# Kernel tuning notes

Hardware: AMD Instinct MI355X
Metric: run time of the kernel (lower is better)

The kernel has to match this reference:

```python
import jax, jax.numpy as jnp
import numpy as np

N_HEAD = 12

def setup_inputs() -> dict:
    key = jax.random.key(0)
    k1, k2, k3, k4, k5 = jax.random.split(key, 5)
    B, T, C = 2, 2048, 768
    x = jax.random.normal(k1, (B, T, C), dtype=jnp.float32)
    W_attn = jax.random.normal(k2, (C, 3 * C), dtype=jnp.float32) * 0.02
    b_attn = jax.random.normal(k3, (3 * C,), dtype=jnp.float32) * 0.02
    W_proj = jax.random.normal(k4, (C, C), dtype=jnp.float32) * 0.02
    b_proj = jax.random.normal(k5, (C,), dtype=jnp.float32) * 0.02
    return {"x": x, "W_attn": W_attn, "b_attn": b_attn, "W_proj": W_proj, "b_proj": b_proj}

def reference(x, W_attn, b_attn, W_proj, b_proj):
    B, T, C = x.shape
    H = N_HEAD
    hd = C // H
    qkv = x @ W_attn + b_attn  # [B,T,3C]
    q, k, v = jnp.split(qkv, 3, axis=2)
    # [B,H,T,hd]
    q = q.reshape(B, T, H, hd).transpose(0, 2, 1, 3)
    k = k.reshape(B, T, H, hd).transpose(0, 2, 1, 3)
    v = v.reshape(B, T, H, hd).transpose(0, 2, 1, 3)
    att = jnp.einsum('bhqd,bhkd->bhqk', q, k) / jnp.sqrt(jnp.float32(hd))
    causal = jnp.tril(jnp.ones((T, T), dtype=bool))
    att = jnp.where(causal[None, None], att, -jnp.inf)
    att = jax.nn.softmax(att, axis=-1)
    y = jnp.einsum('bhqk,bhkd->bhqd', att, v)  # [B,H,T,hd]
    y = y.transpose(0, 2, 1, 3).reshape(B, T, C)
    return y @ W_proj + b_proj
```

## Files before the change

kernel.cpp:

```cpp
#include <hip/hip_runtime.h>
#include <stdint.h>

typedef unsigned short u16;
typedef __attribute__((ext_vector_type(8))) short bf16x8;
typedef __attribute__((ext_vector_type(4))) float f32x4;

__device__ __forceinline__ u16 f2bf(float f){
  union { float f; uint32_t u; } v; v.f = f;
  uint32_t u = v.u;
  u += 0x7FFFu + ((u >> 16) & 1u);
  return (u16)(u >> 16);
}

__device__ __forceinline__ float fexp2(float x){
#if __has_builtin(__builtin_amdgcn_exp2f)
  return __builtin_amdgcn_exp2f(x);
#else
  return exp2f(x);
#endif
}

__device__ __forceinline__ uint32_t cvtpk_bf16(float lo, float hi){
  uint32_t d;
  asm("v_cvt_pk_bf16_f32 %0, %1, %2" : "=v"(d) : "v"(lo), "v"(hi));
  return d;
}

__device__ __forceinline__ f32x4 mfma_bf16(bf16x8 a, bf16x8 b, f32x4 c){
  return __builtin_amdgcn_mfma_f32_16x16x32_bf16(a, b, c, 0, 0, 0);
}

#define QSCALE 0.1803368801111244f

__global__ __launch_bounds__(256) void cast_x_k(const float* __restrict__ x,
                                                u16* __restrict__ xb, int n4){
  int i = blockIdx.x*256 + threadIdx.x;
  if (i >= n4) return;
  float4 v = reinterpret_cast<const float4*>(x)[i];
  uint2 o;
  o.x = (uint32_t)f2bf(v.x) | ((uint32_t)f2bf(v.y) << 16);
  o.y = (uint32_t)f2bf(v.z) | ((uint32_t)f2bf(v.w) << 16);
  reinterpret_cast<uint2*>(xb)[i] = o;
}

__global__ __launch_bounds__(256) void transpose_cast_k(const float* __restrict__ in,
                                                        u16* __restrict__ out,
                                                        int R, int C){
  __shared__ u16 tile[64][66];
  int c0 = blockIdx.x*64, r0 = blockIdx.y*64;
  int tc = threadIdx.x & 63, t4 = threadIdx.x >> 6;
  #pragma unroll
  for (int i=0;i<16;i++){ int r = t4 + i*4; tile[r][tc] = f2bf(in[(size_t)(r0+r)*C + c0 + tc]); }
  __syncthreads();
  #pragma unroll
  for (int i=0;i<16;i++){ int cc = t4 + i*4; out[(size_t)(c0+cc)*R + r0 + tc] = tile[tc][cc]; }
}

#define LDP 40

template<int MFRAG>
__global__ __launch_bounds__(256) void gemm_bf16_k(
    const u16* __restrict__ A, const u16* __restrict__ Bt,
    int M, int N, int K, const float* __restrict__ bias, int mode,
    u16* __restrict__ qo, u16* __restrict__ ko, u16* __restrict__ vo,
    float* __restrict__ fo)
{
  constexpr int BM = MFRAG*32;
  __shared__ u16 As[BM*LDP];
  __shared__ u16 Bs[128*LDP];
  const int m0 = blockIdx.y*BM, n0 = blockIdx.x*128;
  const int tid = threadIdx.x, lane = tid & 63, wid = tid >> 6;
  const int lr = lane & 15, lg = lane >> 4;
  const int wr = wid >> 1, wc = wid & 1;
  f32x4 acc[MFRAG][4] = {};
  const int nk = K >> 5;
  for (int kk = 0; kk < nk; ++kk){
    #pragma unroll
    for (int s = 0; s < MFRAG/2; ++s){
      int ci = tid + 256*s;
      int row = ci >> 2, ch = ci & 3;
      *(uint4*)&As[row*LDP + ch*8] = *(const uint4*)&A[(size_t)(m0+row)*K + kk*32 + ch*8];
    }
    #pragma unroll
    for (int s = 0; s < 2; ++s){
      int ci = tid + 256*s;
      int row = ci >> 2, ch = ci & 3;
      *(uint4*)&Bs[row*LDP + ch*8] = *(const uint4*)&Bt[(size_t)(n0+row)*K + kk*32 + ch*8];
    }
    __syncthreads();
    bf16x8 af[MFRAG], bfr[4];
    #pragma unroll
    for (int m=0;m<MFRAG;m++) af[m] = *(const bf16x8*)&As[(wr*(MFRAG*16) + m*16 + lr)*LDP + lg*8];
    #pragma unroll
    for (int n=0;n<4;n++) bfr[n] = *(const bf16x8*)&Bs[(wc*64 + n*16 + lr)*LDP + lg*8];
    #pragma unroll
    for (int m=0;m<MFRAG;m++)
      #pragma unroll
      for (int n=0;n<4;n++)
        acc[m][n] = mfma_bf16(af[m], bfr[n], acc[m][n]);
    __syncthreads();
  }
  if (mode == 0){
    #pragma unroll
    for (int m=0;m<MFRAG;m++)
      #pragma unroll
      for (int n=0;n<4;n++){
        int gn = n0 + wc*64 + n*16 + lr;
        float bv = bias[gn];
        #pragma unroll
        for (int r=0;r<4;r++){
          int gm = m0 + wr*(MFRAG*16) + m*16 + lg*4 + r;
          fo[(size_t)gm*N + gn] = acc[m][n][r] + bv;
        }
      }
  } else {
    int which = n0 / 768;
    u16* dst = (which==0) ? qo : ko;
    float sc = (which==0) ? QSCALE : 1.0f;
    #pragma unroll
    for (int m=0;m<MFRAG;m++)
      #pragma unroll
      for (int n=0;n<4;n++){
        int gn = n0 + wc*64 + n*16 + lr;
        float bv = bias[gn];
        int cn = gn - which*768;
        int h = cn >> 6, d = cn & 63;
        int gm0 = m0 + wr*(MFRAG*16) + m*16 + lg*4;
        int b = gm0 >> 11, t0 = gm0 & 2047;
        if (which < 2){
          #pragma unroll
          for (int r=0;r<4;r++)
            dst[(size_t)((b*12 + h)*2048 + t0 + r)*64 + d] = f2bf((acc[m][n][r] + bv)*sc);
        } else {
          uint2 o;
          o.x = cvtpk_bf16(acc[m][n][0]+bv, acc[m][n][1]+bv);
          o.y = cvtpk_bf16(acc[m][n][2]+bv, acc[m][n][3]+bv);
          *(uint2*)&vo[((size_t)((b*12 + h)*64 + d))*2048 + t0] = o;
        }
      }
  }
}

__global__ __launch_bounds__(256) void attn_k(
    const u16* __restrict__ qp, const u16* __restrict__ kp,
    const u16* __restrict__ vtp, u16* __restrict__ yp)
{
  __shared__ f32x4 ylh[16][64];
  __shared__ float llh[4][16];
  const int i = blockIdx.x;
  const int bh = i % 24;
  const int qsb = 31 - (i / 24);
  const int q0 = qsb * 64;
  const int b = bh / 12, h = bh - b*12;
  const size_t base = (size_t)bh * 131072;
  const int tid = threadIdx.x, lane = tid & 63, wid = tid >> 6;
  const int lr = lane & 15, lg = lane >> 4;
  const u16* kbase = kp + base;
  const u16* vbase = vtp + base;

  bf16x8 qf0[2], qf1[2], qf2[2], qf3[2];
  #pragma unroll
  for (int kb=0;kb<2;kb++){
    qf0[kb] = *(const bf16x8*)&qp[base + (size_t)(q0      + lr)*64 + kb*32 + lg*8];
    qf1[kb] = *(const bf16x8*)&qp[base + (size_t)(q0 + 16 + lr)*64 + kb*32 + lg*8];
    qf2[kb] = *(const bf16x8*)&qp[base + (size_t)(q0 + 32 + lr)*64 + kb*32 + lg*8];
    qf3[kb] = *(const bf16x8*)&qp[base + (size_t)(q0 + 48 + lr)*64 + kb*32 + lg*8];
  }

  f32x4 y0[4] = {}, y1[4] = {}, y2[4] = {}, y3[4] = {};
  float l0 = 0.f, l1 = 0.f, l2 = 0.f, l3 = 0.f;
  const float m2 = 8.f;
  const int nt = qsb + 1;

  uint32_t ko[8], vo[8];
  #pragma unroll
  for (int nb=0;nb<4;nb++){
    int ke = ((nb&1)*32 + (lr>>2)*8 + (nb>>1)*4 + (lr&3))*64 + lg*8;
    ko[nb*2+0] = (uint32_t)(wid*4096 + ke) * 2u;
    ko[nb*2+1] = (uint32_t)(wid*4096 + ke + 32) * 2u;
  }
  #pragma unroll
  for (int n=0;n<4;n++){
    int ve = (n*16+lr)*2048 + lg*8 + wid*64;
    vo[n*2+0] = (uint32_t)ve * 2u;
    vo[n*2+1] = (uint32_t)(ve + 32) * 2u;
  }

  for (int t = wid; t < nt; t += 4){
    bf16x8 kf[8], vf[8];
    #pragma unroll
    for (int j=0;j<8;j++) kf[j] = *(const bf16x8*)((const char*)kbase + ko[j]);
    #pragma unroll
    for (int j=0;j<8;j++) vf[j] = *(const bf16x8*)((const char*)vbase + vo[j]);
    #pragma unroll
    for (int j=0;j<8;j++){ ko[j] += 32768u; vo[j] += 512u; }

    const int k0 = t*64;
    const int nbmin[4] = {0, 32, 4, 36};

    auto do_half = [&](int q0H, const bf16x8 (&qfH)[2], f32x4 (&yH)[4], float &lH){
      const int qgH = q0H + lr;
      f32x4 s[4] = {};
      __builtin_amdgcn_s_setprio(1);
      if (k0      <= q0H + 15){ s[0]=mfma_bf16(kf[0],qfH[0],s[0]); s[0]=mfma_bf16(kf[1],qfH[1],s[0]); }
      if (k0 + 32 <= q0H + 15){ s[1]=mfma_bf16(kf[2],qfH[0],s[1]); s[1]=mfma_bf16(kf[3],qfH[1],s[1]); }
      if (k0 +  4 <= q0H + 15){ s[2]=mfma_bf16(kf[4],qfH[0],s[2]); s[2]=mfma_bf16(kf[5],qfH[1],s[2]); }
      if (k0 + 36 <= q0H + 15){ s[3]=mfma_bf16(kf[6],qfH[0],s[3]); s[3]=mfma_bf16(kf[7],qfH[1],s[3]); }
      __builtin_amdgcn_s_setprio(0);
      if (k0 + 63 > q0H){
        #pragma unroll
        for (int nb=0;nb<4;nb++){
          int kb0 = k0 + (nb&1)*32 + ((nb>>1)&1)*4 + lg*8;
          #pragma unroll
          for (int r=0;r<4;r++)
            if (kb0 + r > qgH) s[nb][r] = -1e30f;
        }
      }
      float lsum = 0.f;
      #pragma unroll
      for (int nb=0;nb<4;nb++){
        if (k0 + nbmin[nb] <= q0H + 15){
          #pragma unroll
          for (int r=0;r<4;r++){
            float p = fexp2(s[nb][r] - m2);
            s[nb][r] = p;
            lsum += p;
          }
        } else {
          #pragma unroll
          for (int r=0;r<4;r++) s[nb][r] = 0.f;
        }
      }
      lH += lsum;
      uint32_t pk[8];
      #pragma unroll
      for (int nb=0;nb<4;nb++){
        pk[nb*2]   = cvtpk_bf16(s[nb][0], s[nb][1]);
        pk[nb*2+1] = cvtpk_bf16(s[nb][2], s[nb][3]);
      }
      __builtin_amdgcn_s_setprio(1);
      union { uint32_t u[4]; bf16x8 v; } pb;
      pb.u[0]=pk[0]; pb.u[1]=pk[1]; pb.u[2]=pk[4]; pb.u[3]=pk[5];
      yH[0]=mfma_bf16(vf[0],pb.v,yH[0]); yH[1]=mfma_bf16(vf[2],pb.v,yH[1]);
      yH[2]=mfma_bf16(vf[4],pb.v,yH[2]); yH[3]=mfma_bf16(vf[6],pb.v,yH[3]);
      pb.u[0]=pk[2]; pb.u[1]=pk[3]; pb.u[2]=pk[6]; pb.u[3]=pk[7];
      yH[0]=mfma_bf16(vf[1],pb.v,yH[0]); yH[1]=mfma_bf16(vf[3],pb.v,yH[1]);
      yH[2]=mfma_bf16(vf[5],pb.v,yH[2]); yH[3]=mfma_bf16(vf[7],pb.v,yH[3]);
      __builtin_amdgcn_s_setprio(0);
    };
    do_half(q0     , qf0, y0, l0);
    do_half(q0 + 16, qf1, y1, l1);
    do_half(q0 + 32, qf2, y2, l2);
    do_half(q0 + 48, qf3, y3, l3);
  }

  l0 += __shfl_xor(l0, 16);  l0 += __shfl_xor(l0, 32);
  l1 += __shfl_xor(l1, 16);  l1 += __shfl_xor(l1, 32);
  l2 += __shfl_xor(l2, 16);  l2 += __shfl_xor(l2, 32);
  l3 += __shfl_xor(l3, 16);  l3 += __shfl_xor(l3, 32);

  auto phase = [&](const f32x4 (&yH)[4], float lH, int hf){
    if (hf) __syncthreads();
    #pragma unroll
    for (int n=0;n<4;n++) ylh[wid*4+n][lane] = yH[n];
    if (lg == 0) llh[wid][lr] = lH;
    __syncthreads();
    float Ls = (llh[0][lr] + llh[1][lr]) + (llh[2][lr] + llh[3][lr]);
    f32x4 a0 = ylh[0*4+wid][lane], a1 = ylh[1*4+wid][lane],
          a2 = ylh[2*4+wid][lane], a3 = ylh[3*4+wid][lane];
    f32x4 ys;
    #pragma unroll
    for (int r=0;r<4;r++) ys[r] = (a0[r] + a1[r]) + (a2[r] + a3[r]);
    float inv = 1.0f / Ls;
    uint2 o;
    o.x = cvtpk_bf16(ys[0]*inv, ys[1]*inv);
    o.y = cvtpk_bf16(ys[2]*inv, ys[3]*inv);
    *(uint2*)&yp[(size_t)(b*2048 + q0 + hf*16 + lr)*768 + h*64 + wid*16 + lg*4] = o;
  };
  phase(y0, l0, 0);
  phase(y1, l1, 1);
  phase(y2, l2, 2);
  phase(y3, l3, 3);
}

extern "C" void kernel_launch(void* const* d_in, const int* in_sizes, int n_in,
                              void* d_out, int out_size, void* d_ws, size_t ws_size,
                              hipStream_t stream)
{
  const float* x  = (const float*)d_in[0];
  const float* Wa = (const float*)d_in[1];
  const float* ba = (const float*)d_in[2];
  const float* Wp = (const float*)d_in[3];
  const float* bp = (const float*)d_in[4];
  float* out = (float*)d_out;
  char* ws = (char*)d_ws;
  u16* xb  = (u16*)(ws + 0);
  u16* wt  = (u16*)(ws + 6291456);
  u16* wpt = (u16*)(ws + 9830400);
  u16* qb  = (u16*)(ws + 11010048);
  u16* kb  = (u16*)(ws + 17301504);
  u16* vtb = (u16*)(ws + 23592960);
  u16* yb  = (u16*)(ws + 29884416);

  cast_x_k<<<3072, 256, 0, stream>>>(x, xb, 786432);
  transpose_cast_k<<<dim3(36,12), 256, 0, stream>>>(Wa, wt, 768, 2304);
  transpose_cast_k<<<dim3(12,12), 256, 0, stream>>>(Wp, wpt, 768, 768);
  gemm_bf16_k<2><<<dim3(18,64), 256, 0, stream>>>(xb, wt, 4096, 2304, 768, ba, 1,
                                                  qb, kb, vtb, nullptr);
  attn_k<<<768, 256, 0, stream>>>(qb, kb, vtb, yb);
  gemm_bf16_k<2><<<dim3(6,64), 256, 0, stream>>>(yb, wpt, 4096, 768, 768, bp, 0,
                                                 nullptr, nullptr, nullptr, out);
}
```

Before: 121.9 us.

## Pair high and low 32-row query blocks per workgroup to balance causal work

Each workgroup now handles two 32-row query blocks, one from the end of the sequence and one from the start, instead of one 64-row block. Key tiles for both blocks are enumerated in a single combined loop across the four waves, so every workgroup processes roughly the same number of tiles (33). This is meant to remove the load imbalance of the causal triangle, where late query blocks did far more work than early ones. In exchange each key/value tile is now loaded for only 32 query rows, which halves the reuse per load and adds per-iteration branching.

```diff
diff --git a/kernel.cpp b/kernel.cpp
--- a/kernel.cpp
+++ b/kernel.cpp
@@ -149,8 +149,9 @@
   __shared__ float llh[4][16];
   const int i = blockIdx.x;
   const int bh = i % 24;
-  const int qsb = 31 - (i / 24);
-  const int q0 = qsb * 64;
+  const int pr = i / 24;
+  const int qbH = 63 - pr, qbL = pr;
+  const int q0H = qbH * 32, q0L = qbL * 32;
   const int b = bh / 12, h = bh - b*12;
   const size_t base = (size_t)bh * 131072;
   const int tid = threadIdx.x, lane = tid & 63, wid = tid >> 6;
@@ -158,68 +159,70 @@
   const u16* kbase = kp + base;
   const u16* vbase = vtp + base;
 
-  bf16x8 qf0[2], qf1[2], qf2[2], qf3[2];
+  bf16x8 qH0[2], qH1[2], qL0[2], qL1[2];
   #pragma unroll
   for (int kb=0;kb<2;kb++){
-    qf0[kb] = *(const bf16x8*)&qp[base + (size_t)(q0      + lr)*64 + kb*32 + lg*8];
-    qf1[kb] = *(const bf16x8*)&qp[base + (size_t)(q0 + 16 + lr)*64 + kb*32 + lg*8];
-    qf2[kb] = *(const bf16x8*)&qp[base + (size_t)(q0 + 32 + lr)*64 + kb*32 + lg*8];
-    qf3[kb] = *(const bf16x8*)&qp[base + (size_t)(q0 + 48 + lr)*64 + kb*32 + lg*8];
+    qH0[kb] = *(const bf16x8*)&qp[base + (size_t)(q0H      + lr)*64 + kb*32 + lg*8];
+    qH1[kb] = *(const bf16x8*)&qp[base + (size_t)(q0H + 16 + lr)*64 + kb*32 + lg*8];
+    qL0[kb] = *(const bf16x8*)&qp[base + (size_t)(q0L      + lr)*64 + kb*32 + lg*8];
+    qL1[kb] = *(const bf16x8*)&qp[base + (size_t)(q0L + 16 + lr)*64 + kb*32 + lg*8];
   }
 
-  f32x4 y0[4] = {}, y1[4] = {}, y2[4] = {}, y3[4] = {};
-  float l0 = 0.f, l1 = 0.f, l2 = 0.f, l3 = 0.f;
+  f32x4 yH0[4] = {}, yH1[4] = {}, yL0[4] = {}, yL1[4] = {};
+  float lH0 = 0.f, lH1 = 0.f, lL0 = 0.f, lL1 = 0.f;
   const float m2 = 8.f;
-  const int nt = qsb + 1;
-
-  uint32_t ko[8], vo[8];
-  #pragma unroll
-  for (int nb=0;nb<4;nb++){
-    int ke = ((nb&1)*32 + (lr>>2)*8 + (nb>>1)*4 + (lr&3))*64 + lg*8;
-    ko[nb*2+0] = (uint32_t)(wid*4096 + ke) * 2u;
-    ko[nb*2+1] = (uint32_t)(wid*4096 + ke + 32) * 2u;
-  }
-  #pragma unroll
-  for (int n=0;n<4;n++){
-    int ve = (n*16+lr)*2048 + lg*8 + wid*64;
-    vo[n*2+0] = (uint32_t)ve * 2u;
-    vo[n*2+1] = (uint32_t)(ve + 32) * 2u;
-  }
-
-  for (int t = wid; t < nt; t += 4){
+  const int ntH = (qbH >> 1) + 1;
+
+  uint32_t klane[4], vlane[4];
+  #pragma unroll
+  for (int nb=0;nb<4;nb++)
+    klane[nb] = (uint32_t)(((nb&1)*32 + (lr>>2)*8 + (nb>>1)*4 + (lr&3))*64 + lg*8)*2u;
+  #pragma unroll
+  for (int n=0;n<4;n++)
+    vlane[n] = (uint32_t)((n*16+lr)*2048 + lg*8)*2u;
+
+  for (int j = wid; j < 33; j += 4){
+    const bool isH = (j < ntH);
+    const int t = isH ? j : j - ntH;
+    const int k0 = t*64;
+
     bf16x8 kf[8], vf[8];
     #pragma unroll
-    for (int j=0;j<8;j++) kf[j] = *(const bf16x8*)((const char*)kbase + ko[j]);
-    #pragma unroll
-    for (int j=0;j<8;j++) vf[j] = *(const bf16x8*)((const char*)vbase + vo[j]);
-    #pragma unroll
-    for (int j=0;j<8;j++){ ko[j] += 32768u; vo[j] += 512u; }
-
-    const int k0 = t*64;
+    for (int nb=0;nb<4;nb++){
+      uint32_t ko = (uint32_t)t*8192u + klane[nb];
+      kf[nb*2+0] = *(const bf16x8*)((const char*)kbase + ko);
+      kf[nb*2+1] = *(const bf16x8*)((const char*)kbase + ko + 64u);
+    }
+    #pragma unroll
+    for (int n=0;n<4;n++){
+      uint32_t vo = (uint32_t)t*128u + vlane[n];
+      vf[n*2+0] = *(const bf16x8*)((const char*)vbase + vo);
+      vf[n*2+1] = *(const bf16x8*)((const char*)vbase + vo + 64u);
+    }
+
     const int nbmin[4] = {0, 32, 4, 36};
-
-    auto do_half = [&](int q0H, const bf16x8 (&qfH)[2], f32x4 (&yH)[4], float &lH){
-      const int qgH = q0H + lr;
+    auto do_half = [&](int q0X, const bf16x8 (&qfX)[2], f32x4 (&yX)[4], float &lX){
+      const int qgX = q0X + lr;
       f32x4 s[4] = {};
       __builtin_amdgcn_s_setprio(1);
-      if (k0      <= q0H + 15){ s[0]=mfma_bf16(kf[0],qfH[0],s[0]); s[0]=mfma_bf16(kf[1],qfH[1],s[0]); }
-      if (k0 + 32 <= q0H + 15){ s[1]=mfma_bf16(kf[2],qfH[0],s[1]); s[1]=mfma_bf16(kf[3],qfH[1],s[1]); }
-      if (k0 +  4 <= q0H + 15){ s[2]=mfma_bf16(kf[4],qfH[0],s[2]); s[2]=mfma_bf16(kf[5],qfH[1],s[2]); }
-      if (k0 + 36 <= q0H + 15){ s[3]=mfma_bf16(kf[6],qfH[0],s[3]); s[3]=mfma_bf16(kf[7],qfH[1],s[3]); }
+      if (k0      <= q0X + 15){ s[0]=mfma_bf16(kf[0],qfX[0],s[0]); s[0]=mfma_bf16(kf[1],qfX[1],s[0]); }
+      if (k0 + 32 <= q0X + 15){ s[1]=mfma_bf16(kf[2],qfX[0],s[1]); s[1]=mfma_bf16(kf[3],qfX[1],s[1]); }
+      if (k0 +  4 <= q0X + 15){ s[2]=mfma_bf16(kf[4],qfX[0],s[2]); s[2]=mfma_bf16(kf[5],qfX[1],s[2]); }
+      if (k0 + 36 <= q0X + 15){ s[3]=mfma_bf16(kf[6],qfX[0],s[3]); s[3]=mfma_bf16(kf[7],qfX[1],s[3]); }
       __builtin_amdgcn_s_setprio(0);
-      if (k0 + 63 > q0H){
+      if (k0 + 63 > q0X){
         #pragma unroll
         for (int nb=0;nb<4;nb++){
           int kb0 = k0 + (nb&1)*32 + ((nb>>1)&1)*4 + lg*8;
           #pragma unroll
           for (int r=0;r<4;r++)
-            if (kb0 + r > qgH) s[nb][r] = -1e30f;
+            if (kb0 + r > qgX) s[nb][r] = -1e30f;
         }
       }
       float lsum = 0.f;
       #pragma unroll
       for (int nb=0;nb<4;nb++){
-        if (k0 + nbmin[nb] <= q0H + 15){
+        if (k0 + nbmin[nb] <= q0X + 15){
           #pragma unroll
           for (int r=0;r<4;r++){
             float p = fexp2(s[nb][r] - m2);
@@ -231,7 +234,7 @@
           for (int r=0;r<4;r++) s[nb][r] = 0.f;
         }
       }
-      lH += lsum;
+      lX += lsum;
       uint32_t pk[8];
       #pragma unroll
       for (int nb=0;nb<4;nb++){
@@ -241,29 +244,32 @@
       __builtin_amdgcn_s_setprio(1);
       union { uint32_t u[4]; bf16x8 v; } pb;
       pb.u[0]=pk[0]; pb.u[1]=pk[1]; pb.u[2]=pk[4]; pb.u[3]=pk[5];
-      yH[0]=mfma_bf16(vf[0],pb.v,yH[0]); yH[1]=mfma_bf16(vf[2],pb.v,yH[1]);
-      yH[2]=mfma_bf16(vf[4],pb.v,yH[2]); yH[3]=mfma_bf16(vf[6],pb.v,yH[3]);
+      yX[0]=mfma_bf16(vf[0],pb.v,yX[0]); yX[1]=mfma_bf16(vf[2],pb.v,yX[1]);
+      yX[2]=mfma_bf16(vf[4],pb.v,yX[2]); yX[3]=mfma_bf16(vf[6],pb.v,yX[3]);
       pb.u[0]=pk[2]; pb.u[1]=pk[3]; pb.u[2]=pk[6]; pb.u[3]=pk[7];
-      yH[0]=mfma_bf16(vf[1],pb.v,yH[0]); yH[1]=mfma_bf16(vf[3],pb.v,yH[1]);
-      yH[2]=mfma_bf16(vf[5],pb.v,yH[2]); yH[3]=mfma_bf16(vf[7],pb.v,yH[3]);
+      yX[0]=mfma_bf16(vf[1],pb.v,yX[0]); yX[1]=mfma_bf16(vf[3],pb.v,yX[1]);
+      yX[2]=mfma_bf16(vf[5],pb.v,yX[2]); yX[3]=mfma_bf16(vf[7],pb.v,yX[3]);
       __builtin_amdgcn_s_setprio(0);
     };
-    do_half(q0     , qf0, y0, l0);
-    do_half(q0 + 16, qf1, y1, l1);
-    do_half(q0 + 32, qf2, y2, l2);
-    do_half(q0 + 48, qf3, y3, l3);
+    if (isH){
+      do_half(q0H     , qH0, yH0, lH0);
+      do_half(q0H + 16, qH1, yH1, lH1);
+    } else {
+      do_half(q0L     , qL0, yL0, lL0);
+      do_half(q0L + 16, qL1, yL1, lL1);
+    }
   }
 
-  l0 += __shfl_xor(l0, 16);  l0 += __shfl_xor(l0, 32);
-  l1 += __shfl_xor(l1, 16);  l1 += __shfl_xor(l1, 32);
-  l2 += __shfl_xor(l2, 16);  l2 += __shfl_xor(l2, 32);
-  l3 += __shfl_xor(l3, 16);  l3 += __shfl_xor(l3, 32);
-
-  auto phase = [&](const f32x4 (&yH)[4], float lH, int hf){
-    if (hf) __syncthreads();
-    #pragma unroll
-    for (int n=0;n<4;n++) ylh[wid*4+n][lane] = yH[n];
-    if (lg == 0) llh[wid][lr] = lH;
+  lH0 += __shfl_xor(lH0, 16);  lH0 += __shfl_xor(lH0, 32);
+  lH1 += __shfl_xor(lH1, 16);  lH1 += __shfl_xor(lH1, 32);
+  lL0 += __shfl_xor(lL0, 16);  lL0 += __shfl_xor(lL0, 32);
+  lL1 += __shfl_xor(lL1, 16);  lL1 += __shfl_xor(lL1, 32);
+
+  auto phase = [&](const f32x4 (&yX)[4], float lX, int qrow0, int first){
+    if (!first) __syncthreads();
+    #pragma unroll
+    for (int n=0;n<4;n++) ylh[wid*4+n][lane] = yX[n];
+    if (lg == 0) llh[wid][lr] = lX;
     __syncthreads();
     float Ls = (llh[0][lr] + llh[1][lr]) + (llh[2][lr] + llh[3][lr]);
     f32x4 a0 = ylh[0*4+wid][lane], a1 = ylh[1*4+wid][lane],
@@ -275,12 +281,12 @@
     uint2 o;
     o.x = cvtpk_bf16(ys[0]*inv, ys[1]*inv);
     o.y = cvtpk_bf16(ys[2]*inv, ys[3]*inv);
-    *(uint2*)&yp[(size_t)(b*2048 + q0 + hf*16 + lr)*768 + h*64 + wid*16 + lg*4] = o;
+    *(uint2*)&yp[(size_t)(b*2048 + qrow0 + lr)*768 + h*64 + wid*16 + lg*4] = o;
   };
-  phase(y0, l0, 0);
-  phase(y1, l1, 1);
-  phase(y2, l2, 2);
-  phase(y3, l3, 3);
+  phase(yH0, lH0, q0H     , 1);
+  phase(yH1, lH1, q0H + 16, 0);
+  phase(yL0, lL0, q0L     , 0);
+  phase(yL1, lL1, q0L + 16, 0);
 }
 
 extern "C" void kernel_launch(void* const* d_in, const int* in_sizes, int n_in,
```

Result: slower. 132.0 us (+8.3%).
